# Kernel optimization log

Measured on AMD Instinct MI355X. Metric: run time of the kernel, lower is better.

The kernel has to match this reference:

```python
import jax, jax.numpy as jnp
import numpy as np
from jax import lax

D = 256      # key/query dim
D_F = 256    # diff feature channels
C_TOK = 1    # leading context tokens in query_vit
EPS = 1e-6


def conv2d(x, w, b, pad):
    out = lax.conv_general_dilated(x, w, (1, 1), [(pad, pad), (pad, pad)],
                                   dimension_numbers=('NCHW', 'OIHW', 'NCHW'))
    return out + b[None, :, None, None]


def gn1(x, g, b):
    # GroupNorm with 1 group: normalize over (C,H,W) per sample
    mu = jnp.mean(x, axis=(1, 2, 3), keepdims=True)
    var = jnp.var(x, axis=(1, 2, 3), keepdims=True)
    xn = (x - mu) * lax.rsqrt(var + EPS)
    return xn * g[None, :, None, None] + b[None, :, None, None]


def resize_bilinear_ac(x, Ho, Wo):
    # F.interpolate(mode='bilinear', align_corners=True)
    B, C, H, W = x.shape
    ys = jnp.linspace(0.0, H - 1.0, Ho)
    xs = jnp.linspace(0.0, W - 1.0, Wo)
    y0 = jnp.floor(ys).astype(jnp.int32)
    y1 = jnp.minimum(y0 + 1, H - 1)
    wy = (ys - y0)[None, None, :, None]
    x0 = jnp.floor(xs).astype(jnp.int32)
    x1 = jnp.minimum(x0 + 1, W - 1)
    wx = (xs - x0)[None, None, None, :]
    r = x[:, :, y0, :] * (1.0 - wy) + x[:, :, y1, :] * wy
    return r[:, :, :, x0] * (1.0 - wx) + r[:, :, :, x1] * wx


def setup_inputs() -> dict:
    key = jax.random.key(0)
    ks = jax.random.split(key, 12)
    B, Hd, Wd, Ht, Wt = 8, 64, 64, 32, 32

    def kaiming(k, shape, fan_in):
        return jax.random.normal(k, shape, jnp.float32) * np.sqrt(2.0 / fan_in)

    return {
        'query_vit': jax.random.normal(ks[0], (B, C_TOK + Ht * Wt, D), jnp.float32),
        'feat_diff_cat': jax.random.normal(ks[1], (B, 5 * D_F, Hd, Wd), jnp.float32),
        'rb_w1': kaiming(ks[2], (D_F, 5 * D_F, 3, 3), 5 * D_F * 9), 'rb_b1': jnp.zeros((D_F,), jnp.float32),
        'rb_w2': kaiming(ks[3], (D_F, D_F, 3, 3), D_F * 9), 'rb_b2': jnp.zeros((D_F,), jnp.float32),
        'rb_ws': kaiming(ks[4], (D_F, 5 * D_F, 1, 1), 5 * D_F), 'rb_bs': jnp.zeros((D_F,), jnp.float32),
        'ln_g': jnp.ones((D_F,), jnp.float32), 'ln_b': jnp.zeros((D_F,), jnp.float32),
        'key_w': kaiming(ks[5], (D, D_F, 1, 1), D_F), 'key_b': jnp.zeros((D,), jnp.float32),
        'val_w': kaiming(ks[6], (D_F, D_F, 1, 1), D_F), 'val_b': jnp.zeros((D_F,), jnp.float32),
        'dh0_w': kaiming(ks[7], (D_F, D_F, 3, 3), D_F * 9), 'dh0_b': jnp.zeros((D_F,), jnp.float32),
        'dh1_w': kaiming(ks[8], (D_F, D_F, 3, 3), D_F * 9), 'dh1_b': jnp.zeros((D_F,), jnp.float32),
    }


def reference(query_vit, feat_diff_cat, rb_w1, rb_b1, rb_w2, rb_b2, rb_ws, rb_bs,
              ln_g, ln_b, key_w, key_b, val_w, val_b, dh0_w, dh0_b, dh1_w, dh1_b):
    B, _, h_diff, w_diff = feat_diff_cat.shape
    N = query_vit.shape[1] - C_TOK
    h_trm = w_trm = int(N ** 0.5)

    # ResBlock_ysh(D_f*5 -> D_f): conv3x3 + relu + conv3x3, 1x1-projected residual
    h = jax.nn.relu(conv2d(feat_diff_cat, rb_w1, rb_b1, 1))
    h = conv2d(h, rb_w2, rb_b2, 1)
    feat_diff = jax.nn.relu(h + conv2d(feat_diff_cat, rb_ws, rb_bs, 0))

    fln = gn1(feat_diff, ln_g, ln_b)
    key_diff = conv2d(fln, key_w, key_b, 0).reshape(B, D, -1)          # (B, D, HW)
    value_diff = conv2d(fln, val_w, val_b, 0).reshape(B, D_F, -1)      # (B, Df, HW)
    value_diff = jnp.transpose(value_diff, (0, 2, 1))                  # (B, HW, Df)

    # cross attention: (B, C+N, D) @ (B, D, HW) -> softmax -> @ (B, HW, Df)
    scores = jnp.einsum('bnd,bdm->bnm', query_vit, key_diff) * (D ** -0.5)
    attn = jax.nn.softmax(scores, axis=-1)
    out_cross = jnp.einsum('bnm,bmf->bnf', attn, value_diff)           # (B, C+N, Df)

    out_cross_c = out_cross[:, :C_TOK, :]
    out_p = jnp.transpose(out_cross[:, C_TOK:, :], (0, 2, 1)).reshape(B, D_F, h_trm, w_trm)
    out_p = jax.nn.relu(conv2d(out_p, dh0_w, dh0_b, 1))
    out_p = resize_bilinear_ac(out_p, h_diff, w_diff)
    out_p = out_p + feat_diff                                          # DropPath(0) = identity
    out_p = jax.nn.relu(conv2d(gn1(out_p, ln_g, ln_b), dh1_w, dh1_b, 1)) + out_p
    return out_cross_c, out_p
```

## Files before the change

kernel.cpp:

```cpp
#include <hip/hip_runtime.h>
#include <cstdint>
#include <cstddef>

typedef __attribute__((ext_vector_type(4))) float     f32x4;
typedef __attribute__((ext_vector_type(8))) __bf16    bf16x8;
typedef __attribute__((ext_vector_type(8))) short     short8;
typedef __attribute__((ext_vector_type(4))) unsigned short u16x4;
typedef unsigned short u16;

__device__ __forceinline__ float b2f(u16 u) {
  unsigned x = ((unsigned)u) << 16;
  float f;
  __builtin_memcpy(&f, &x, 4);
  return f;
}
__device__ __forceinline__ u16 f2b(float f) {
  unsigned u;
  __builtin_memcpy(&u, &f, 4);
  return (u16)((u + 0x7FFFu + ((u >> 16) & 1u)) >> 16);
}

struct GP {
  const u16*  A;
  const u16*  B;
  const float* bias;
  const void* aux;
  void*       C;
  float*      out0;
  long long   aBS, bBS, cBS, auxBS;
  int Ktot, Mrows, ldc;
  int cin, logW, wpad, poff;
  float scale;
};

#define GLDS16(g, l)                                                        \
  __builtin_amdgcn_global_load_lds(                                         \
      (const void __attribute__((address_space(1)))*)(g),                   \
      (void __attribute__((address_space(3)))*)(l), 16, 0, 0)

template <int AMODE, int CW, bool RELU>
__global__ __launch_bounds__(256, 2) void k_gemm(GP gp) {
  const int tid = threadIdx.x;
  const int l = tid & 63, w = tid >> 6;
  const int b = blockIdx.z;
  const int m0 = blockIdx.x * 128, n0 = blockIdx.y * 128;
  const int wm = w >> 1, wn = w & 1;

  __shared__ __align__(16) u16 smA[128 * 64];
  __shared__ __align__(16) u16 smB[128 * 64];

  f32x4 acc[4][4];
#pragma unroll
  for (int i = 0; i < 4; ++i)
#pragma unroll
    for (int j = 0; j < 4; ++j) acc[i][j] = (f32x4){0.f, 0.f, 0.f, 0.f};

  const u16* Ab = gp.A + (size_t)b * gp.aBS;
  const u16* Bb = gp.B + (size_t)b * gp.bBS;

  const int scoff = (((l & 7) ^ (l >> 3)) << 3);

  const u16* aRow[4];
  const u16* bRow[4];
  u16* ldsA[4];
  u16* ldsB[4];
#pragma unroll
  for (int i = 0; i < 4; ++i) {
    const int r = w * 32 + i * 8 + (l >> 3);
    bRow[i] = Bb + (size_t)(n0 + r) * gp.Ktot + scoff;
    const int p = m0 + r;
    if (AMODE == 0) {
      const int pc = p < gp.Mrows ? p : gp.Mrows - 1;
      aRow[i] = Ab + (size_t)pc * gp.Ktot + scoff;
    } else {
      const int y = p >> gp.logW, x = p & ((1 << gp.logW) - 1);
      const int icoord = (y + gp.poff) * gp.wpad + (x + gp.poff);
      aRow[i] = Ab + (size_t)icoord * gp.cin + scoff;
    }
    ldsA[i] = smA + (w * 32 + i * 8) * 64;
    ldsB[i] = smB + (w * 32 + i * 8) * 64;
  }

  const int ktiles = gp.Ktot >> 6;
  int tap_off = 0, dx = 0, kc = 0;

  for (int kt = 0; kt < ktiles; ++kt) {
    int koffA;
    if (AMODE == 0)
      koffA = kt << 6;
    else
      koffA = tap_off * gp.cin + kc;
    const int koffB = kt << 6;
#pragma unroll
    for (int i = 0; i < 4; ++i) GLDS16(aRow[i] + koffA, ldsA[i]);
#pragma unroll
    for (int i = 0; i < 4; ++i) GLDS16(bRow[i] + koffB, ldsB[i]);

    if (AMODE == 1) {
      kc += 64;
      if (kc == gp.cin) {
        kc = 0;
        ++dx;
        ++tap_off;
        if (dx == 3) { dx = 0; tap_off += gp.wpad - 3; }
      }
    }

    __syncthreads();
#pragma unroll
    for (int ks = 0; ks < 2; ++ks) {
      bf16x8 av[4], bv[4];
      const int cc = (ks << 2) + (l >> 4);
#pragma unroll
      for (int mi = 0; mi < 4; ++mi) {
        const int row = wm * 64 + mi * 16 + (l & 15);
        av[mi] = *(const bf16x8*)((const char*)smA + (row << 7) +
                                  ((cc ^ (row & 7)) << 4));
      }
#pragma unroll
      for (int ni = 0; ni < 4; ++ni) {
        const int row = wn * 64 + ni * 16 + (l & 15);
        bv[ni] = *(const bf16x8*)((const char*)smB + (row << 7) +
                                  ((cc ^ (row & 7)) << 4));
      }
#pragma unroll
      for (int mi = 0; mi < 4; ++mi)
#pragma unroll
        for (int ni = 0; ni < 4; ++ni)
          acc[mi][ni] = __builtin_amdgcn_mfma_f32_16x16x32_bf16(
              av[mi], bv[ni], acc[mi][ni], 0, 0, 0);
    }
    __syncthreads();
  }

#pragma unroll
  for (int mi = 0; mi < 4; ++mi) {
#pragma unroll
    for (int ni = 0; ni < 4; ++ni) {
      const int ncol = n0 + wn * 64 + ni * 16 + (l & 15);
      const int mbase = m0 + wm * 64 + mi * 16 + ((l >> 4) << 2);
      const float bv_ = gp.bias ? gp.bias[ncol] : 0.f;

      if constexpr (CW == 3) {
        u16* Cu = (u16*)gp.C + (size_t)b * gp.cBS + (size_t)ncol * 4096 + mbase;
        u16x4 pk;
#pragma unroll
        for (int r = 0; r < 4; ++r) pk[r] = f2b(acc[mi][ni][r] + bv_);
        *(u16x4*)Cu = pk;
      } else if constexpr (CW == 6) {
        float* Cf = (float*)gp.C + (size_t)b * gp.cBS + (size_t)ncol * 4096 + mbase;
        const float* mid = (const float*)gp.aux + (size_t)b * gp.auxBS;
        f32x4 o;
#pragma unroll
        for (int r = 0; r < 4; ++r) {
          float v = acc[mi][ni][r] + bv_;
          v = v > 0.f ? v : 0.f;
          o[r] = v + mid[(size_t)(mbase + r) * 256 + ncol];
        }
        *(f32x4*)Cf = o;
      } else {
#pragma unroll
        for (int reg = 0; reg < 4; ++reg) {
          const int mrow = mbase + reg;
          if (mrow >= gp.Mrows) continue;
          float v = acc[mi][ni][reg] * gp.scale + bv_;
          if (RELU) v = v > 0.f ? v : 0.f;
          if constexpr (CW == 0) {
            ((u16*)gp.C)[(size_t)b * gp.cBS + (size_t)mrow * gp.ldc + ncol] =
                f2b(v);
          } else if constexpr (CW == 1) {
            const int y = mrow >> 6, x = mrow & 63;
            ((u16*)gp.C)[(size_t)b * gp.cBS +
                         (size_t)((y + 1) * 66 + (x + 1)) * 256 + ncol] = f2b(v);
          } else if constexpr (CW == 2) {
            const float s =
                b2f(((const u16*)gp.aux)[(size_t)b * gp.auxBS +
                                         (size_t)mrow * 256 + ncol]);
            float v2 = v + s;
            v2 = v2 > 0.f ? v2 : 0.f;
            ((float*)gp.C)[(size_t)b * gp.cBS + (size_t)mrow * 256 + ncol] = v2;
          } else if constexpr (CW == 4) {
            if (mrow == 0) {
              gp.out0[(size_t)b * 256 + ncol] = v;
            } else {
              const int p = mrow - 1, y = p >> 5, x = p & 31;
              ((u16*)gp.C)[(size_t)b * gp.cBS +
                           (size_t)((y + 1) * 34 + (x + 1)) * 256 + ncol] =
                  f2b(v);
            }
          } else if constexpr (CW == 5) {
            ((float*)gp.C)[(size_t)b * gp.cBS + (size_t)mrow * 256 + ncol] = v;
          }
        }
      }
    }
  }
}


__global__ __launch_bounds__(256) void k_prep_x(const float* __restrict__ x,
                                                u16* __restrict__ o) {
  __shared__ float t[32][65];
  const int b = blockIdx.z, c0 = blockIdx.y << 5, y = blockIdx.x;
  const float* src = x + ((size_t)b * 1280 + c0) * 4096 + (size_t)y * 64;
#pragma unroll
  for (int i = 0; i < 8; ++i) {
    const int idx = threadIdx.x + (i << 8);
    const int c = idx >> 6, xx = idx & 63;
    t[c][xx] = src[(size_t)c * 4096 + xx];
  }
  __syncthreads();
  u16* dst = o + ((size_t)b * 4356 + (size_t)(y + 1) * 66 + 1) * 1280 + c0;
#pragma unroll
  for (int i = 0; i < 8; ++i) {
    const int idx = threadIdx.x + (i << 8);
    const int xx = idx >> 5, c = idx & 31;
    dst[(size_t)xx * 1280 + c] = f2b(t[c][xx]);
  }
}

__global__ __launch_bounds__(256) void k_prep_w3(const float* __restrict__ w,
                                                 u16* __restrict__ o, int cin,
                                                 int n) {
  for (int i = blockIdx.x * 256 + threadIdx.x; i < n; i += gridDim.x * 256) {
    const int ci = i % cin;
    const int r = i / cin;
    const int t = r % 9;
    const int co = r / 9;
    o[i] = f2b(w[((size_t)co * cin + ci) * 9 + t]);
  }
}

__global__ __launch_bounds__(256) void k_f2b(const float* __restrict__ x,
                                             u16* __restrict__ o, int n) {
  for (int i = blockIdx.x * 256 + threadIdx.x; i < n; i += gridDim.x * 256)
    o[i] = f2b(x[i]);
}

__global__ __launch_bounds__(256) void k_gn_stats(const float* __restrict__ x,
                                                  float* __restrict__ st) {
  const int b = blockIdx.y;
  const f32x4* xb = (const f32x4*)(x + (size_t)b * 1048576);
  float s = 0.f, s2 = 0.f;
  for (int i = blockIdx.x * 256 + threadIdx.x; i < 262144;
       i += gridDim.x * 256) {
    const f32x4 v = xb[i];
    s += v[0] + v[1] + v[2] + v[3];
    s2 += v[0] * v[0] + v[1] * v[1] + v[2] * v[2] + v[3] * v[3];
  }
#pragma unroll
  for (int o = 32; o; o >>= 1) {
    s += __shfl_down(s, o);
    s2 += __shfl_down(s2, o);
  }
  __shared__ float ls[4], ls2[4];
  const int w = threadIdx.x >> 6;
  if ((threadIdx.x & 63) == 0) { ls[w] = s; ls2[w] = s2; }
  __syncthreads();
  if (threadIdx.x == 0) {
    atomicAdd(&st[b * 2], ls[0] + ls[1] + ls[2] + ls[3]);
    atomicAdd(&st[b * 2 + 1], ls2[0] + ls2[1] + ls2[2] + ls2[3]);
  }
}

template <bool PAD>
__global__ __launch_bounds__(256) void k_gn_norm(const float* __restrict__ x,
                                                 const float* __restrict__ st,
                                                 const float* __restrict__ g,
                                                 const float* __restrict__ bb,
                                                 u16* __restrict__ o) {
  const int b = blockIdx.y;
  const float mu = st[b * 2] * (1.f / 1048576.f);
  const float var = st[b * 2 + 1] * (1.f / 1048576.f) - mu * mu;
  const float rs = rsqrtf(var + 1e-6f);
  const int i4 = blockIdx.x * 256 + threadIdx.x;
  const f32x4 v = ((const f32x4*)(x + (size_t)b * 1048576))[i4];
  const int flat = i4 << 2;
  const int c = flat & 255;
  const int p = flat >> 8;
  const f32x4 gv = *(const f32x4*)(g + c);
  const f32x4 bv = *(const f32x4*)(bb + c);
  u16x4 r;
#pragma unroll
  for (int k = 0; k < 4; ++k) r[k] = f2b((v[k] - mu) * rs * gv[k] + bv[k]);
  size_t oidx;
  if (PAD) {
    const int y = p >> 6, xx = p & 63;
    oidx = ((size_t)b * 4356 + (size_t)(y + 1) * 66 + xx + 1) * 256 + c;
  } else {
    oidx = ((size_t)b * 4096 + p) * 256 + c;
  }
  *(u16x4*)(o + oidx) = r;
}

__global__ __launch_bounds__(256) void k_softmax(u16* __restrict__ s) {
  const size_t row = blockIdx.x;
  u16* p = s + row * 4096;
  const int t = threadIdx.x;
  const short8 r0 = ((const short8*)p)[t];
  const short8 r1 = ((const short8*)p)[t + 256];
  float v[16];
#pragma unroll
  for (int i = 0; i < 8; ++i) {
    v[i] = b2f((u16)r0[i]);
    v[8 + i] = b2f((u16)r1[i]);
  }
  float m = v[0];
#pragma unroll
  for (int i = 1; i < 16; ++i) m = fmaxf(m, v[i]);
#pragma unroll
  for (int o = 32; o; o >>= 1) m = fmaxf(m, __shfl_xor(m, o));
  __shared__ float lm[4], lsum[4];
  const int w = t >> 6;
  if ((t & 63) == 0) lm[w] = m;
  __syncthreads();
  m = fmaxf(fmaxf(lm[0], lm[1]), fmaxf(lm[2], lm[3]));
  float sum = 0.f;
#pragma unroll
  for (int i = 0; i < 16; ++i) {
    v[i] = __expf(v[i] - m);
    sum += v[i];
  }
#pragma unroll
  for (int o = 32; o; o >>= 1) sum += __shfl_xor(sum, o);
  if ((t & 63) == 0) lsum[w] = sum;
  __syncthreads();
  sum = lsum[0] + lsum[1] + lsum[2] + lsum[3];
  const float inv = 1.f / sum;
  short8 o0, o1;
#pragma unroll
  for (int i = 0; i < 8; ++i) {
    o0[i] = (short)f2b(v[i] * inv);
    o1[i] = (short)f2b(v[8 + i] * inv);
  }
  ((short8*)p)[t] = o0;
  ((short8*)p)[t + 256] = o1;
}

__global__ __launch_bounds__(256) void k_resize_add(const float* __restrict__ d0,
                                                    const float* __restrict__ F,
                                                    float* __restrict__ mid) {
  const int i4 = blockIdx.x * 256 + threadIdx.x;
  const int flat = i4 << 2;
  const int c = flat & 255;
  const int p = (flat >> 8) & 4095;
  const int b = flat >> 20;
  const int y = p >> 6, x = p & 63;
  const float fy = y * (31.f / 63.f);
  const int y0 = (int)fy;
  const float wy = fy - y0;
  const int y1 = y0 + 1 > 31 ? 31 : y0 + 1;
  const float fx = x * (31.f / 63.f);
  const int x0 = (int)fx;
  const float wx = fx - x0;
  const int x1 = x0 + 1 > 31 ? 31 : x0 + 1;
  const float* db = d0 + (size_t)b * 262144;
  const f32x4 a = *(const f32x4*)(db + ((size_t)(y0 * 32 + x0) << 8) + c);
  const f32x4 bq = *(const f32x4*)(db + ((size_t)(y0 * 32 + x1) << 8) + c);
  const f32x4 cq = *(const f32x4*)(db + ((size_t)(y1 * 32 + x0) << 8) + c);
  const f32x4 dq = *(const f32x4*)(db + ((size_t)(y1 * 32 + x1) << 8) + c);
  f32x4 r = (a * (1.f - wx) + bq * wx) * (1.f - wy) +
            (cq * (1.f - wx) + dq * wx) * wy;
  r += *(const f32x4*)(F + (size_t)flat);
  *(f32x4*)(mid + (size_t)flat) = r;
}


extern "C" void kernel_launch(void* const* d_in, const int* in_sizes, int n_in,
                              void* d_out, int out_size, void* d_ws,
                              size_t ws_size, hipStream_t stream) {
  (void)in_sizes; (void)n_in; (void)out_size;

  const float* q   = (const float*)d_in[0];
  const float* xdc = (const float*)d_in[1];
  const float* w1  = (const float*)d_in[2];
  const float* b1  = (const float*)d_in[3];
  const float* w2  = (const float*)d_in[4];
  const float* b2  = (const float*)d_in[5];
  const float* wsc = (const float*)d_in[6];
  const float* bsc = (const float*)d_in[7];
  const float* lng = (const float*)d_in[8];
  const float* lnb = (const float*)d_in[9];
  const float* wk  = (const float*)d_in[10];
  const float* bk  = (const float*)d_in[11];
  const float* wv  = (const float*)d_in[12];
  const float* bv  = (const float*)d_in[13];
  const float* wd0 = (const float*)d_in[14];
  const float* bd0 = (const float*)d_in[15];
  const float* wd1 = (const float*)d_in[16];
  const float* bd1 = (const float*)d_in[17];

  char* ws = (char*)d_ws;
  size_t cur = 0;
  auto alloc = [&](size_t sz) {
    char* p = ws + cur;
    cur += sz;
    return p;
  };
  u16* XPAD = (u16*)alloc(89194496);
  u16* W1R  = (u16*)alloc(5898240);
  u16* W2R  = (u16*)alloc(1179648);
  u16* WSR  = (u16*)alloc(655360);
  u16* WKR  = (u16*)alloc(131072);
  u16* WVR  = (u16*)alloc(131072);
  u16* WD0R = (u16*)alloc(1179648);
  u16* WD1R = (u16*)alloc(1179648);
  u16* SB   = (u16*)alloc(16777216);
  u16* H1   = (u16*)alloc(17842176);
  float* F  = (float*)alloc(33554432);
  u16* FLN  = (u16*)alloc(16777216);
  u16* KT   = (u16*)alloc(16777216);
  u16* V    = (u16*)alloc(16777216);
  u16* QB   = (u16*)alloc(4198400);
  u16* OCP  = (u16*)alloc(4734976);
  float* D0O = (float*)alloc(8388608);
  float* MID = (float*)alloc(33554432);
  u16* G2   = (u16*)alloc(17842176);
  float* ST = (float*)alloc(256);
  u16* SCORES = XPAD;

  if (ws_size < cur) return;

  float* out0 = (float*)d_out;
  float* out1 = (float*)d_out + 2048;

  hipMemsetAsync(XPAD, 0, 89194496, stream);
  hipMemsetAsync(H1, 0, 17842176, stream);
  hipMemsetAsync(OCP, 0, 4734976, stream);
  hipMemsetAsync(G2, 0, 17842176, stream);
  hipMemsetAsync(ST, 0, 256, stream);

  k_prep_x<<<dim3(64, 40, 8), 256, 0, stream>>>(xdc, XPAD);
  k_prep_w3<<<2048, 256, 0, stream>>>(w1, W1R, 1280, 2949120);
  k_prep_w3<<<1024, 256, 0, stream>>>(w2, W2R, 256, 589824);
  k_prep_w3<<<1024, 256, 0, stream>>>(wd0, WD0R, 256, 589824);
  k_prep_w3<<<1024, 256, 0, stream>>>(wd1, WD1R, 256, 589824);
  k_f2b<<<512, 256, 0, stream>>>(wsc, WSR, 327680);
  k_f2b<<<128, 256, 0, stream>>>(wk, WKR, 65536);
  k_f2b<<<128, 256, 0, stream>>>(wv, WVR, 65536);
  k_f2b<<<2048, 256, 0, stream>>>(q, QB, 2099200);

  {
    GP g{};
    g.A = XPAD; g.B = WSR; g.bias = bsc; g.C = SB;
    g.aBS = 5575680; g.bBS = 0; g.cBS = 1048576;
    g.Ktot = 1280; g.Mrows = 4096; g.ldc = 256;
    g.cin = 1280; g.logW = 6; g.wpad = 66; g.poff = 1; g.scale = 1.f;
    k_gemm<1, 0, false><<<dim3(32, 2, 8), 256, 0, stream>>>(g);
  }
  {
    GP g{};
    g.A = XPAD; g.B = W1R; g.bias = b1; g.C = H1;
    g.aBS = 5575680; g.bBS = 0; g.cBS = 1115136;
    g.Ktot = 11520; g.Mrows = 4096; g.ldc = 256;
    g.cin = 1280; g.logW = 6; g.wpad = 66; g.poff = 0; g.scale = 1.f;
    k_gemm<1, 1, true><<<dim3(32, 2, 8), 256, 0, stream>>>(g);
  }
  {
    GP g{};
    g.A = H1; g.B = W2R; g.bias = b2; g.C = F; g.aux = SB;
    g.aBS = 1115136; g.bBS = 0; g.cBS = 1048576; g.auxBS = 1048576;
    g.Ktot = 2304; g.Mrows = 4096; g.ldc = 256;
    g.cin = 256; g.logW = 6; g.wpad = 66; g.poff = 0; g.scale = 1.f;
    k_gemm<1, 2, false><<<dim3(32, 2, 8), 256, 0, stream>>>(g);
  }
  k_gn_stats<<<dim3(64, 8), 256, 0, stream>>>(F, ST);
  k_gn_norm<false><<<dim3(1024, 8), 256, 0, stream>>>(F, ST, lng, lnb, FLN);
  {
    GP g{};
    g.A = FLN; g.B = WKR; g.bias = bk; g.C = KT;
    g.aBS = 1048576; g.bBS = 0; g.cBS = 1048576;
    g.Ktot = 256; g.Mrows = 4096; g.ldc = 256; g.scale = 1.f;
    k_gemm<0, 0, false><<<dim3(32, 2, 8), 256, 0, stream>>>(g);
  }
  {
    GP g{};
    g.A = FLN; g.B = WVR; g.bias = bv; g.C = V;
    g.aBS = 1048576; g.bBS = 0; g.cBS = 1048576;
    g.Ktot = 256; g.Mrows = 4096; g.ldc = 256; g.scale = 1.f;
    k_gemm<0, 3, false><<<dim3(32, 2, 8), 256, 0, stream>>>(g);
  }
  {
    GP g{};
    g.A = QB; g.B = KT; g.bias = nullptr; g.C = SCORES;
    g.aBS = 262400; g.bBS = 1048576; g.cBS = 4198400;
    g.Ktot = 256; g.Mrows = 1025; g.ldc = 4096; g.scale = 0.0625f;
    k_gemm<0, 0, false><<<dim3(9, 32, 8), 256, 0, stream>>>(g);
  }
  k_softmax<<<8200, 256, 0, stream>>>(SCORES);
  {
    GP g{};
    g.A = SCORES; g.B = V; g.bias = nullptr; g.C = OCP; g.out0 = out0;
    g.aBS = 4198400; g.bBS = 1048576; g.cBS = 295936;
    g.Ktot = 4096; g.Mrows = 1025; g.ldc = 256; g.scale = 1.f;
    k_gemm<0, 4, false><<<dim3(9, 2, 8), 256, 0, stream>>>(g);
  }
  {
    GP g{};
    g.A = OCP; g.B = WD0R; g.bias = bd0; g.C = D0O;
    g.aBS = 295936; g.bBS = 0; g.cBS = 262144;
    g.Ktot = 2304; g.Mrows = 1024; g.ldc = 256;
    g.cin = 256; g.logW = 5; g.wpad = 34; g.poff = 0; g.scale = 1.f;
    k_gemm<1, 5, true><<<dim3(8, 2, 8), 256, 0, stream>>>(g);
  }
  k_resize_add<<<8192, 256, 0, stream>>>(D0O, F, MID);
  k_gn_stats<<<dim3(64, 8), 256, 0, stream>>>(MID, ST + 16);
  k_gn_norm<true><<<dim3(1024, 8), 256, 0, stream>>>(MID, ST + 16, lng, lnb, G2);
  {
    GP g{};
    g.A = G2; g.B = WD1R; g.bias = bd1; g.C = out1; g.aux = MID;
    g.aBS = 1115136; g.bBS = 0; g.cBS = 1048576; g.auxBS = 1048576;
    g.Ktot = 2304; g.Mrows = 4096; g.ldc = 256;
    g.cin = 256; g.logW = 6; g.wpad = 66; g.poff = 0; g.scale = 1.f;
    k_gemm<1, 6, false><<<dim3(32, 2, 8), 256, 0, stream>>>(g);
  }
}
```

Baseline: 760.9 us.

## Add 512-thread full-N GEMM with triple-buffered LDS, fuse K/V projections, zero only borders

Adds k_gemm8, a 512-thread kernel that computes a 128x256 tile covering the full N=256 per block. It uses a three-stage LDS pipeline with split loads, setprio and sched barriers, and replaces the 128x128 GEMM for the four conv layers. The key and value 1x1 projections are merged into one GEMM with concatenated weights and biases, and the full-buffer memsets are replaced by a kernel that zeroes only the padded borders. The aim is to reuse the A tile across all of N, overlap loads with MFMA, and cut redundant memset traffic, at the cost of fewer blocks per grid (256) and higher LDS use per block.

Result: faster. 743.7 us (-2.3%).

```diff
diff --git a/kernel.cpp b/kernel.cpp
--- a/kernel.cpp
+++ b/kernel.cpp
@@ -39,6 +39,230 @@
       (void __attribute__((address_space(3)))*)(l), 16, 0, 0)
 
 template <int AMODE, int CW, bool RELU>
+__global__ __launch_bounds__(512, 2) void k_gemm8(GP gp) {
+  const int tid = threadIdx.x;
+  const int l = tid & 63, w = tid >> 6;
+  const int b = blockIdx.z;
+  const int m0 = blockIdx.x * 128;
+  const int wm = w >> 2, wn = w & 3;
+
+  __shared__ __align__(16) u16 sm[3][24576];
+
+  f32x4 acc[4][4];
+#pragma unroll
+  for (int i = 0; i < 4; ++i)
+#pragma unroll
+    for (int j = 0; j < 4; ++j) acc[i][j] = (f32x4){0.f, 0.f, 0.f, 0.f};
+
+  const u16* Ab = gp.A + (size_t)b * gp.aBS;
+  const u16* Bb = gp.B + (size_t)b * gp.bBS;
+  const int scoff = (((tid & 7) ^ ((tid >> 3) & 7)) << 3);
+
+  const u16* aP[2];
+  const u16* bP[4];
+#pragma unroll
+  for (int i = 0; i < 2; ++i) {
+    const int p = m0 + i * 64 + (tid >> 3);
+    if (AMODE == 0) {
+      const int pc = p < gp.Mrows ? p : gp.Mrows - 1;
+      aP[i] = Ab + (size_t)pc * gp.Ktot + scoff;
+    } else {
+      const int y = p >> gp.logW, x = p & ((1 << gp.logW) - 1);
+      aP[i] = Ab + (size_t)((y + gp.poff) * gp.wpad + (x + gp.poff)) * gp.cin +
+              scoff;
+    }
+  }
+#pragma unroll
+  for (int i = 0; i < 4; ++i)
+    bP[i] = Bb + (size_t)(i * 64 + (tid >> 3)) * gp.Ktot + scoff;
+
+  const int NT = gp.Ktot >> 6;
+  int kcS = 0, tapS = 0, dxS = 0, ktS = 0;
+
+  auto adv = [&](int& kA, int& kB) {
+    kB = ktS << 6;
+    if (AMODE == 0) {
+      kA = ktS << 6;
+    } else {
+      kA = tapS * gp.cin + kcS;
+      kcS += 64;
+      if (kcS == gp.cin) {
+        kcS = 0; ++dxS; ++tapS;
+        if (dxS == 3) { dxS = 0; tapS += gp.wpad - 3; }
+      }
+    }
+    ++ktS;
+  };
+
+#pragma unroll
+  for (int pt = 0; pt < 2; ++pt) {
+    int kA, kB;
+    adv(kA, kB);
+    u16* sA = &sm[pt][0] + (w << 9);
+    u16* sB = &sm[pt][8192] + (w << 9);
+    GLDS16(aP[0] + kA, sA);
+    GLDS16(aP[1] + kA, sA + 4096);
+    GLDS16(bP[0] + kB, sB);
+    GLDS16(bP[1] + kB, sB + 4096);
+    GLDS16(bP[2] + kB, sB + 8192);
+    GLDS16(bP[3] + kB, sB + 12288);
+  }
+  asm volatile("s_waitcnt vmcnt(6)" ::: "memory");
+  __builtin_amdgcn_s_barrier();
+
+  const int lr = l & 15, lc = l >> 4;
+  int bufC = 0, bufS = 2;
+
+  for (int t = 0; t < NT; ++t) {
+    const u16* sAc = &sm[bufC][0];
+    const u16* sBc = &sm[bufC][8192];
+    const bool sOK = (t + 2 < NT);
+    int kAs = 0, kBs = 0;
+    if (sOK) adv(kAs, kBs);
+    u16* sAs = &sm[bufS][0] + (w << 9);
+    u16* sBs = &sm[bufS][8192] + (w << 9);
+
+    bf16x8 bv[4][2];
+    {
+      bf16x8 av[2][2];
+#pragma unroll
+      for (int mi = 0; mi < 2; ++mi) {
+        const int row = wm * 64 + mi * 16 + lr;
+#pragma unroll
+        for (int ks = 0; ks < 2; ++ks) {
+          const int cc = ks * 4 + lc;
+          av[mi][ks] =
+              *(const bf16x8*)(sAc + row * 64 + ((cc ^ (row & 7)) << 3));
+        }
+      }
+#pragma unroll
+      for (int ni = 0; ni < 4; ++ni) {
+        const int row = wn * 64 + ni * 16 + lr;
+#pragma unroll
+        for (int ks = 0; ks < 2; ++ks) {
+          const int cc = ks * 4 + lc;
+          bv[ni][ks] =
+              *(const bf16x8*)(sBc + row * 64 + ((cc ^ (row & 7)) << 3));
+        }
+      }
+      if (sOK) {
+        GLDS16(aP[0] + kAs, sAs);
+        GLDS16(aP[1] + kAs, sAs + 4096);
+        GLDS16(bP[0] + kBs, sBs);
+      }
+      __builtin_amdgcn_s_barrier();
+      asm volatile("s_waitcnt lgkmcnt(0)" ::: "memory");
+      __builtin_amdgcn_sched_barrier(0);
+      __builtin_amdgcn_s_setprio(1);
+#pragma unroll
+      for (int ks = 0; ks < 2; ++ks)
+#pragma unroll
+        for (int mi = 0; mi < 2; ++mi)
+#pragma unroll
+          for (int ni = 0; ni < 4; ++ni)
+            acc[mi][ni] = __builtin_amdgcn_mfma_f32_16x16x32_bf16(
+                av[mi][ks], bv[ni][ks], acc[mi][ni], 0, 0, 0);
+      __builtin_amdgcn_sched_barrier(0);
+      __builtin_amdgcn_s_setprio(0);
+    }
+    __builtin_amdgcn_s_barrier();
+    {
+      bf16x8 av[2][2];
+#pragma unroll
+      for (int mi = 0; mi < 2; ++mi) {
+        const int row = wm * 64 + (mi + 2) * 16 + lr;
+#pragma unroll
+        for (int ks = 0; ks < 2; ++ks) {
+          const int cc = ks * 4 + lc;
+          av[mi][ks] =
+              *(const bf16x8*)(sAc + row * 64 + ((cc ^ (row & 7)) << 3));
+        }
+      }
+      if (sOK) {
+        GLDS16(bP[1] + kBs, sBs + 4096);
+        GLDS16(bP[2] + kBs, sBs + 8192);
+        GLDS16(bP[3] + kBs, sBs + 12288);
+      }
+      __builtin_amdgcn_s_barrier();
+      asm volatile("s_waitcnt lgkmcnt(0)" ::: "memory");
+      __builtin_amdgcn_sched_barrier(0);
+      __builtin_amdgcn_s_setprio(1);
+#pragma unroll
+      for (int ks = 0; ks < 2; ++ks)
+#pragma unroll
+        for (int mi = 0; mi < 2; ++mi)
+#pragma unroll
+          for (int ni = 0; ni < 4; ++ni)
+            acc[mi + 2][ni] = __builtin_amdgcn_mfma_f32_16x16x32_bf16(
+                av[mi][ks], bv[ni][ks], acc[mi + 2][ni], 0, 0, 0);
+      __builtin_amdgcn_sched_barrier(0);
+      __builtin_amdgcn_s_setprio(0);
+    }
+    if (t + 1 < NT) {
+      if (t + 2 < NT)
+        asm volatile("s_waitcnt vmcnt(6)" ::: "memory");
+      else
+        asm volatile("s_waitcnt vmcnt(0)" ::: "memory");
+      __builtin_amdgcn_s_barrier();
+    }
+    bufC = bufC == 2 ? 0 : bufC + 1;
+    bufS = bufS == 2 ? 0 : bufS + 1;
+  }
+
+#pragma unroll
+  for (int mi = 0; mi < 4; ++mi) {
+#pragma unroll
+    for (int ni = 0; ni < 4; ++ni) {
+      const int ncol = wn * 64 + ni * 16 + lr;
+      const int mbase = m0 + wm * 64 + mi * 16 + lc * 4;
+      const float bv_ = gp.bias ? gp.bias[ncol] : 0.f;
+      if constexpr (CW == 0) {
+#pragma unroll
+        for (int r = 0; r < 4; ++r) {
+          float v = acc[mi][ni][r] + bv_;
+          if (RELU) v = fmaxf(v, 0.f);
+          ((u16*)gp.C)[(size_t)b * gp.cBS + (size_t)(mbase + r) * 256 + ncol] =
+              f2b(v);
+        }
+      } else if constexpr (CW == 1) {
+#pragma unroll
+        for (int r = 0; r < 4; ++r) {
+          float v = acc[mi][ni][r] + bv_;
+          if (RELU) v = fmaxf(v, 0.f);
+          const int mrow = mbase + r;
+          const int y = mrow >> 6, x = mrow & 63;
+          ((u16*)gp.C)[(size_t)b * gp.cBS +
+                       (size_t)((y + 1) * 66 + x + 1) * 256 + ncol] = f2b(v);
+        }
+      } else if constexpr (CW == 2) {
+#pragma unroll
+        for (int r = 0; r < 4; ++r) {
+          const int mrow = mbase + r;
+          const float s =
+              b2f(((const u16*)gp.aux)[(size_t)b * gp.auxBS +
+                                       (size_t)mrow * 256 + ncol]);
+          float v = acc[mi][ni][r] + bv_ + s;
+          v = fmaxf(v, 0.f);
+          ((float*)gp.C)[(size_t)b * gp.cBS + (size_t)mrow * 256 + ncol] = v;
+        }
+      } else if constexpr (CW == 6) {
+        float* Cf =
+            (float*)gp.C + (size_t)b * gp.cBS + (size_t)ncol * 4096 + mbase;
+        const float* mid = (const float*)gp.aux + (size_t)b * gp.auxBS;
+        f32x4 o;
+#pragma unroll
+        for (int r = 0; r < 4; ++r) {
+          float v = acc[mi][ni][r] + bv_;
+          v = fmaxf(v, 0.f);
+          o[r] = v + mid[(size_t)(mbase + r) * 256 + ncol];
+        }
+        *(f32x4*)Cf = o;
+      }
+    }
+  }
+}
+
+template <int AMODE, int CW, bool RELU>
 __global__ __launch_bounds__(256, 2) void k_gemm(GP gp) {
   const int tid = threadIdx.x;
   const int l = tid & 63, w = tid >> 6;
@@ -147,6 +371,20 @@
 #pragma unroll
         for (int r = 0; r < 4; ++r) pk[r] = f2b(acc[mi][ni][r] + bv_);
         *(u16x4*)Cu = pk;
+      } else if constexpr (CW == 7) {
+        u16* base = (u16*)gp.C;
+        if (ncol < 256) {
+#pragma unroll
+          for (int r = 0; r < 4; ++r)
+            base[(size_t)b * 1048576 + (size_t)(mbase + r) * 256 + ncol] =
+                f2b(acc[mi][ni][r] + bv_);
+        } else {
+          u16x4 pk;
+#pragma unroll
+          for (int r = 0; r < 4; ++r) pk[r] = f2b(acc[mi][ni][r] + bv_);
+          *(u16x4*)(base + 8388608 + (size_t)b * 1048576 +
+                    (size_t)(ncol - 256) * 4096 + mbase) = pk;
+        }
       } else if constexpr (CW == 6) {
         float* Cf = (float*)gp.C + (size_t)b * gp.cBS + (size_t)ncol * 4096 + mbase;
         const float* mid = (const float*)gp.aux + (size_t)b * gp.auxBS;
@@ -168,10 +406,6 @@
           if constexpr (CW == 0) {
             ((u16*)gp.C)[(size_t)b * gp.cBS + (size_t)mrow * gp.ldc + ncol] =
                 f2b(v);
-          } else if constexpr (CW == 1) {
-            const int y = mrow >> 6, x = mrow & 63;
-            ((u16*)gp.C)[(size_t)b * gp.cBS +
-                         (size_t)((y + 1) * 66 + (x + 1)) * 256 + ncol] = f2b(v);
           } else if constexpr (CW == 2) {
             const float s =
                 b2f(((const u16*)gp.aux)[(size_t)b * gp.auxBS +
@@ -216,6 +450,25 @@
     const int idx = threadIdx.x + (i << 8);
     const int xx = idx >> 5, c = idx & 31;
     dst[(size_t)xx * 1280 + c] = f2b(t[c][xx]);
+  }
+}
+
+__global__ __launch_bounds__(256) void k_zero_border(u16* __restrict__ p,
+                                                     int P, int C) {
+  const int per_img = (4 * P - 4) * C;
+  const int total = 8 * per_img;
+  for (int idx = blockIdx.x * 256 + threadIdx.x; idx < total;
+       idx += gridDim.x * 256) {
+    const int b = idx / per_img;
+    const int r = idx % per_img;
+    const int pix = r / C, c = r % C;
+    int y, x;
+    const int Pm = P - 1;
+    if (pix < P) { y = 0; x = pix; }
+    else if (pix < 2 * P) { y = Pm; x = pix - P; }
+    else if (pix < 3 * P - 2) { y = pix - 2 * P + 1; x = 0; }
+    else { y = pix - (3 * P - 2) + 1; x = Pm; }
+    p[((size_t)b * P * P + (size_t)y * P + x) * C + c] = 0;
   }
 }
 
@@ -401,8 +654,8 @@
   u16* W1R  = (u16*)alloc(5898240);
   u16* W2R  = (u16*)alloc(1179648);
   u16* WSR  = (u16*)alloc(655360);
-  u16* WKR  = (u16*)alloc(131072);
-  u16* WVR  = (u16*)alloc(131072);
+  u16* WKV  = (u16*)alloc(262144);
+  float* BKV = (float*)alloc(2048);
   u16* WD0R = (u16*)alloc(1179648);
   u16* WD1R = (u16*)alloc(1179648);
   u16* SB   = (u16*)alloc(16777216);
@@ -418,17 +671,21 @@
   u16* G2   = (u16*)alloc(17842176);
   float* ST = (float*)alloc(256);
   u16* SCORES = XPAD;
+  (void)V;
 
   if (ws_size < cur) return;
 
   float* out0 = (float*)d_out;
   float* out1 = (float*)d_out + 2048;
 
-  hipMemsetAsync(XPAD, 0, 89194496, stream);
-  hipMemsetAsync(H1, 0, 17842176, stream);
-  hipMemsetAsync(OCP, 0, 4734976, stream);
-  hipMemsetAsync(G2, 0, 17842176, stream);
   hipMemsetAsync(ST, 0, 256, stream);
+  hipMemcpyAsync(BKV, bk, 1024, hipMemcpyDeviceToDevice, stream);
+  hipMemcpyAsync(BKV + 256, bv, 1024, hipMemcpyDeviceToDevice, stream);
+
+  k_zero_border<<<2048, 256, 0, stream>>>(XPAD, 66, 1280);
+  k_zero_border<<<1024, 256, 0, stream>>>(H1, 66, 256);
+  k_zero_border<<<1024, 256, 0, stream>>>(G2, 66, 256);
+  k_zero_border<<<512, 256, 0, stream>>>(OCP, 34, 256);
 
   k_prep_x<<<dim3(64, 40, 8), 256, 0, stream>>>(xdc, XPAD);
   k_prep_w3<<<2048, 256, 0, stream>>>(w1, W1R, 1280, 2949120);
@@ -436,17 +693,18 @@
   k_prep_w3<<<1024, 256, 0, stream>>>(wd0, WD0R, 256, 589824);
   k_prep_w3<<<1024, 256, 0, stream>>>(wd1, WD1R, 256, 589824);
   k_f2b<<<512, 256, 0, stream>>>(wsc, WSR, 327680);
-  k_f2b<<<128, 256, 0, stream>>>(wk, WKR, 65536);
-  k_f2b<<<128, 256, 0, stream>>>(wv, WVR, 65536);
+  k_f2b<<<128, 256, 0, stream>>>(wk, WKV, 65536);
+  k_f2b<<<128, 256, 0, stream>>>(wv, WKV + 65536, 65536);
   k_f2b<<<2048, 256, 0, stream>>>(q, QB, 2099200);
 
+  const dim3 g8(32, 1, 8);
   {
     GP g{};
     g.A = XPAD; g.B = WSR; g.bias = bsc; g.C = SB;
     g.aBS = 5575680; g.bBS = 0; g.cBS = 1048576;
     g.Ktot = 1280; g.Mrows = 4096; g.ldc = 256;
     g.cin = 1280; g.logW = 6; g.wpad = 66; g.poff = 1; g.scale = 1.f;
-    k_gemm<1, 0, false><<<dim3(32, 2, 8), 256, 0, stream>>>(g);
+    k_gemm8<1, 0, false><<<g8, 512, 0, stream>>>(g);
   }
   {
     GP g{};
@@ -454,7 +712,7 @@
     g.aBS = 5575680; g.bBS = 0; g.cBS = 1115136;
     g.Ktot = 11520; g.Mrows = 4096; g.ldc = 256;
     g.cin = 1280; g.logW = 6; g.wpad = 66; g.poff = 0; g.scale = 1.f;
-    k_gemm<1, 1, true><<<dim3(32, 2, 8), 256, 0, stream>>>(g);
+    k_gemm8<1, 1, true><<<g8, 512, 0, stream>>>(g);
   }
   {
     GP g{};
@@ -462,23 +720,16 @@
     g.aBS = 1115136; g.bBS = 0; g.cBS = 1048576; g.auxBS = 1048576;
     g.Ktot = 2304; g.Mrows = 4096; g.ldc = 256;
     g.cin = 256; g.logW = 6; g.wpad = 66; g.poff = 0; g.scale = 1.f;
-    k_gemm<1, 2, false><<<dim3(32, 2, 8), 256, 0, stream>>>(g);
+    k_gemm8<1, 2, false><<<g8, 512, 0, stream>>>(g);
   }
   k_gn_stats<<<dim3(64, 8), 256, 0, stream>>>(F, ST);
   k_gn_norm<false><<<dim3(1024, 8), 256, 0, stream>>>(F, ST, lng, lnb, FLN);
   {
     GP g{};
-    g.A = FLN; g.B = WKR; g.bias = bk; g.C = KT;
-    g.aBS = 1048576; g.bBS = 0; g.cBS = 1048576;
+    g.A = FLN; g.B = WKV; g.bias = BKV; g.C = KT;
+    g.aBS = 1048576; g.bBS = 0; g.cBS = 0;
     g.Ktot = 256; g.Mrows = 4096; g.ldc = 256; g.scale = 1.f;
-    k_gemm<0, 0, false><<<dim3(32, 2, 8), 256, 0, stream>>>(g);
-  }
-  {
-    GP g{};
-    g.A = FLN; g.B = WVR; g.bias = bv; g.C = V;
-    g.aBS = 1048576; g.bBS = 0; g.cBS = 1048576;
-    g.Ktot = 256; g.Mrows = 4096; g.ldc = 256; g.scale = 1.f;
-    k_gemm<0, 3, false><<<dim3(32, 2, 8), 256, 0, stream>>>(g);
+    k_gemm<0, 7, false><<<dim3(32, 4, 8), 256, 0, stream>>>(g);
   }
   {
     GP g{};
@@ -512,6 +763,6 @@
     g.aBS = 1115136; g.bBS = 0; g.cBS = 1048576; g.auxBS = 1048576;
     g.Ktot = 2304; g.Mrows = 4096; g.ldc = 256;
     g.cin = 256; g.logW = 6; g.wpad = 66; g.poff = 0; g.scale = 1.f;
-    k_gemm<1, 6, false><<<dim3(32, 2, 8), 256, 0, stream>>>(g);
-  }
-}
+    k_gemm8<1, 6, false><<<g8, 512, 0, stream>>>(g);
+  }
+}
```
